# Kernel optimization log

Hardware: AMD Instinct MI355X
Metric: run time of the kernel (lower is better)

Reference implementation:

```python
import jax, jax.numpy as jnp
import numpy as np
import math

D_MODEL, N_HEADS, D_FF = 1024, 16, 4096
HEAD_DIM = D_MODEL // N_HEADS
BATCH, SEQ = 2, 2048
POPE_BASE = 10000.0
LN_EPS = 1e-5


def setup_inputs() -> dict:
    key = jax.random.key(0)
    ks = jax.random.split(key, 20)
    s = 0.02
    inp = {
        "x": jax.random.normal(ks[0], (BATCH, SEQ, D_MODEL), dtype=jnp.float32),
        "positions": jnp.arange(SEQ, dtype=jnp.int64) if jax.config.jax_enable_x64 else jnp.arange(SEQ, dtype=jnp.int32),
        "Wq": jax.random.normal(ks[1], (D_MODEL, D_MODEL), jnp.float32) * s,
        "bq": jnp.zeros((D_MODEL,), jnp.float32),
        "Wk": jax.random.normal(ks[2], (D_MODEL, D_MODEL), jnp.float32) * s,
        "bk": jnp.zeros((D_MODEL,), jnp.float32),
        "Wv": jax.random.normal(ks[3], (D_MODEL, D_MODEL), jnp.float32) * s,
        "bv": jnp.zeros((D_MODEL,), jnp.float32),
        "Wo": jax.random.normal(ks[4], (D_MODEL, D_MODEL), jnp.float32) * s,
        "bo": jnp.zeros((D_MODEL,), jnp.float32),
        "phase_bias": jax.random.uniform(ks[5], (N_HEADS, HEAD_DIM), jnp.float32,
                                          minval=-2.0 * math.pi, maxval=0.0),
        "freqs": (1.0 / POPE_BASE ** (jnp.arange(HEAD_DIM, dtype=jnp.float32) / HEAD_DIM)),
        "W1": jax.random.normal(ks[6], (D_MODEL, D_FF), jnp.float32) * s,
        "b1": jnp.zeros((D_FF,), jnp.float32),
        "W2": jax.random.normal(ks[7], (D_FF, D_MODEL), jnp.float32) * s,
        "b2": jnp.zeros((D_MODEL,), jnp.float32),
        "g1": jnp.ones((D_MODEL,), jnp.float32),
        "beta1": jnp.zeros((D_MODEL,), jnp.float32),
        "g2": jnp.ones((D_MODEL,), jnp.float32),
        "beta2": jnp.zeros((D_MODEL,), jnp.float32),
    }
    return inp


def _layernorm(x, g, b):
    mu = jnp.mean(x, axis=-1, keepdims=True)
    var = jnp.mean((x - mu) ** 2, axis=-1, keepdims=True)
    return (x - mu) * jax.lax.rsqrt(var + LN_EPS) * g + b


def reference(x, positions, Wq, bq, Wk, bk, Wv, bv, Wo, bo, phase_bias, freqs,
              W1, b1, W2, b2, g1, beta1, g2, beta2):
    B, S, D = x.shape
    H, hd = N_HEADS, HEAD_DIM

    def split_heads(y):  # (B,S,D) -> (B,H,S,hd)
        return y.reshape(B, S, H, hd).transpose(0, 2, 1, 3)

    q = split_heads(x @ Wq + bq)
    k = split_heads(x @ Wk + bk)
    v = split_heads(x @ Wv + bv)

    # --- PoPE: magnitudes via softplus, phases from positions + learned bias ---
    mu_q = jax.nn.softplus(q)
    mu_k = jax.nn.softplus(k)
    pos_phases = positions[:, None].astype(jnp.float32) * freqs[None, :]        # (S,hd)
    phases = pos_phases[None, None, :, :] + phase_bias[None, :, None, :]        # (1,H,S,hd)
    cosp, sinp = jnp.cos(phases), jnp.sin(phases)
    q_pope = jnp.concatenate([mu_q * cosp, mu_q * sinp], axis=-1)               # (B,H,S,2hd)
    k_pope = jnp.concatenate([mu_k * cosp, mu_k * sinp], axis=-1)

    # --- manual causal attention with softmax1 ---
    scale = 1.0 / math.sqrt(2 * hd)  # q.shape[-1] == 2*head_dim under PoPE
    scores = jnp.einsum("bhsd,bhtd->bhst", q_pope, k_pope) * scale
    causal = jnp.triu(jnp.ones((S, S), dtype=bool), k=1)
    scores = jnp.where(causal[None, None], -jnp.inf, scores)
    m = jnp.max(scores, axis=-1, keepdims=True)
    e = jnp.exp(scores - m)
    attn_w = e / (1.0 + jnp.sum(e, axis=-1, keepdims=True))  # softmax1 (as written in source)
    attn = jnp.einsum("bhst,bhtd->bhsd", attn_w, v)

    attn = attn.transpose(0, 2, 1, 3).reshape(B, S, D) @ Wo + bo
    x = _layernorm(x + attn, g1, beta1)
    ff = jax.nn.relu(x @ W1 + b1) @ W2 + b2
    x = _layernorm(x + ff, g2, beta2)
    return x
```

## Files before the change

### kernel.cpp

```cpp
#include <hip/hip_runtime.h>
#include <hip/hip_bf16.h>
#include <math.h>

#define B_   2
#define S_   2048
#define D_   1024
#define H_   16
#define HD_  64
#define DFF_ 4096
#define M_   (B_*S_)
#define SCALE_ 0.08838834764831845f

typedef __attribute__((ext_vector_type(8))) short bf16x8;
typedef __attribute__((ext_vector_type(4))) float f32x4;

#define MFMA16(a,b,c) __builtin_amdgcn_mfma_f32_16x16x32_bf16((a),(b),(c),0,0,0)

__device__ __forceinline__ unsigned short f2b(float f) {
    union { float f; unsigned u; } v; v.f = f;
    return (unsigned short)((v.u + 0x7FFFu + ((v.u >> 16) & 1u)) >> 16);
}
__device__ __forceinline__ float b2f(unsigned short s) {
    union { unsigned u; float f; } v; v.u = ((unsigned)s) << 16;
    return v.f;
}
__device__ __forceinline__ unsigned pk2bf(float a, float b) {
    union { float f; unsigned u; } ua, ub; ua.f = a; ub.f = b;
    return __builtin_amdgcn_perm(ub.u, ua.u, 0x07060302u);
}
__device__ __forceinline__ float softplus_f(float x) {
    return fmaxf(x, 0.f) + log1pf(__expf(-fabsf(x)));
}
__device__ __forceinline__ void g2l16(const void* g, void* l) {
    __builtin_amdgcn_global_load_lds(
        (const __attribute__((address_space(1))) unsigned int*)g,
        (__attribute__((address_space(3))) unsigned int*)l, 16, 0, 0);
}

__global__ __launch_bounds__(256) void conv_bf16_kernel(
    const float* __restrict__ in, unsigned short* __restrict__ out,
    const float* __restrict__ bq, const float* __restrict__ bk,
    const float* __restrict__ bv, float* __restrict__ bqkv)
{
    int i = (blockIdx.x * 256 + threadIdx.x) * 4;
    float4 v = *(const float4*)&in[i];
    ushort4 o;
    o.x = f2b(v.x); o.y = f2b(v.y); o.z = f2b(v.z); o.w = f2b(v.w);
    *(ushort4*)&out[i] = o;
    int j = blockIdx.x * 256 + threadIdx.x;
    if (j < 3072)
        bqkv[j] = (j < 1024) ? bq[j] : (j < 2048 ? bk[j - 1024] : bv[j - 2048]);
}

__global__ __launch_bounds__(256) void wtrans_kernel(
    const float* __restrict__ W, unsigned short* __restrict__ WT, int K, int N)
{
    __shared__ float tile[32][33];
    const int n0 = blockIdx.x * 32, k0 = blockIdx.y * 32;
    const int tx = threadIdx.x & 31, ty = threadIdx.x >> 5;
    #pragma unroll
    for (int i = 0; i < 4; i++)
        tile[ty + 8*i][tx] = W[(size_t)(k0 + ty + 8*i) * N + n0 + tx];
    __syncthreads();
    #pragma unroll
    for (int i = 0; i < 4; i++)
        WT[(size_t)(n0 + ty + 8*i) * K + k0 + tx] = f2b(tile[tx][ty + 8*i]);
}

__global__ __launch_bounds__(256) void wtrans4_kernel(
    const float* __restrict__ Wa, const float* __restrict__ Wb,
    const float* __restrict__ Wc, const float* __restrict__ Wd,
    unsigned short* __restrict__ Tabc, unsigned short* __restrict__ Td)
{
    __shared__ float tile[32][33];
    const int z = blockIdx.z;
    const float* W = (z == 0) ? Wa : (z == 1) ? Wb : (z == 2) ? Wc : Wd;
    unsigned short* WT = (z < 3) ? Tabc + (size_t)z * 1024 * 1024 : Td;
    const int n0 = blockIdx.x * 32, k0 = blockIdx.y * 32;
    const int tx = threadIdx.x & 31, ty = threadIdx.x >> 5;
    #pragma unroll
    for (int i = 0; i < 4; i++)
        tile[ty + 8*i][tx] = W[(size_t)(k0 + ty + 8*i) * 1024 + n0 + tx];
    __syncthreads();
    #pragma unroll
    for (int i = 0; i < 4; i++)
        WT[(size_t)(n0 + ty + 8*i) * 1024 + k0 + tx] = f2b(tile[tx][ty + 8*i]);
}

__global__ __launch_bounds__(256) void gemm_bf16_kernel(
    const unsigned short* __restrict__ A,
    const unsigned short* __restrict__ WT,
    const float* __restrict__ bias,
    float* __restrict__ outF, unsigned short* __restrict__ outB,
    int M, int Kslice, int lda, int N, int relu)
{
    __shared__ unsigned short As[2][128 * 64];
    __shared__ unsigned short Bs[2][128 * 64];

    const int tid = threadIdx.x;
    const int w = tid >> 6, lane = tid & 63;
    const int quad = lane >> 4, l16 = lane & 15;

    const int nn = gridDim.x, nm = gridDim.y;
    const int lin = ((int)blockIdx.z * nm + (int)blockIdx.y) * nn + (int)blockIdx.x;
    const int per = (nn * nm * (int)gridDim.z) >> 3;
    const int id  = (lin & 7) * per + (lin >> 3);
    const int zz  = id / (nn * nm);
    const int rem = id - zz * nn * nm;
    const int mt_ = rem / nn, nt_ = rem - mt_ * nn;

    const size_t m0 = (size_t)mt_ * 128, n0 = (size_t)nt_ * 128;
    const int wm = (w >> 1) * 64, wn = (w & 1) * 64;
    const int koff = zz * Kslice;

    const int srow = lane >> 3;
    const int sc   = ((lane & 7) ^ srow) * 8;
    const unsigned short* ga = A  + (m0 + w * 32 + srow) * (size_t)lda + koff + sc;
    const unsigned short* gb = WT + (n0 + w * 32 + srow) * (size_t)lda + koff + sc;
    const size_t rows8 = (size_t)8 * lda;

    f32x4 acc[4][4] = {};
    const int niter = Kslice >> 6;

    #pragma unroll
    for (int j = 0; j < 4; j++) g2l16(ga + j * rows8, &As[0][(w * 32 + j * 8) * 64]);
    #pragma unroll
    for (int j = 0; j < 4; j++) g2l16(gb + j * rows8, &Bs[0][(w * 32 + j * 8) * 64]);

    for (int i = 0; i < niter; i++) {
        __syncthreads();
        if (i + 1 < niter) {
            const int nb = (i + 1) & 1, k0 = (i + 1) << 6;
            #pragma unroll
            for (int j = 0; j < 4; j++)
                g2l16(ga + j * rows8 + k0, &As[nb][(w * 32 + j * 8) * 64]);
            #pragma unroll
            for (int j = 0; j < 4; j++)
                g2l16(gb + j * rows8 + k0, &Bs[nb][(w * 32 + j * 8) * 64]);
        }
        const int buf = i & 1;

        #pragma unroll
        for (int kk = 0; kk < 2; kk++) {
            bf16x8 af[4], bfr[4];
            #pragma unroll
            for (int t = 0; t < 4; t++) {
                const int slot = ((kk * 4 + quad) ^ (l16 & 7)) * 8;
                af[t]  = *(const bf16x8*)&As[buf][(wm + t * 16 + l16) * 64 + slot];
                bfr[t] = *(const bf16x8*)&Bs[buf][(wn + t * 16 + l16) * 64 + slot];
            }
            #pragma unroll
            for (int mt = 0; mt < 4; mt++)
                #pragma unroll
                for (int nt = 0; nt < 4; nt++)
                    acc[mt][nt] = MFMA16(af[mt], bfr[nt], acc[mt][nt]);
        }
    }

    float bv[4];
    #pragma unroll
    for (int nt = 0; nt < 4; nt++)
        bv[nt] = (zz == 0) ? bias[n0 + wn + nt * 16 + l16] : 0.f;

    float* outFz = outF ? outF + (size_t)zz * M * N : nullptr;

    #pragma unroll
    for (int mt = 0; mt < 4; mt++) {
        #pragma unroll
        for (int nt = 0; nt < 4; nt++) {
            const size_t n = n0 + wn + nt * 16 + l16;
            #pragma unroll
            for (int r = 0; r < 4; r++) {
                const size_t m = m0 + wm + mt * 16 + quad * 4 + r;
                float val = acc[mt][nt][r] + bv[nt];
                if (relu) val = fmaxf(val, 0.f);
                const size_t idx = m * N + n;
                if (outFz) outFz[idx] = val;
                if (outB) outB[idx] = f2b(val);
            }
        }
    }
}

__global__ __launch_bounds__(256) void pope_kernel(
    const unsigned short* __restrict__ qkv,
    const float* __restrict__ phase_bias, const float* __restrict__ freqs,
    unsigned short* __restrict__ qp, unsigned short* __restrict__ kp)
{
    int idx = blockIdx.x * 256 + threadIdx.x;
    int d = idx & 63;
    int s = (idx >> 6) & (S_ - 1);
    int h = (idx >> 17) & (H_ - 1);
    int b = idx >> 21;

    size_t src = (size_t)(b * S_ + s) * 3072 + h * HD_ + d;
    float muq = softplus_f(b2f(qkv[src])) * SCALE_;
    float muk = softplus_f(b2f(qkv[src + 1024]));

    float ph = (float)s * freqs[d] + phase_bias[h * HD_ + d];
    float sn, cs;
    __sincosf(ph, &sn, &cs);

    size_t o = ((size_t)(b * H_ + h) * S_ + s) * 128 + d;
    qp[o]      = f2b(muq * cs);
    qp[o + 64] = f2b(muq * sn);
    kp[o]      = f2b(muk * cs);
    kp[o + 64] = f2b(muk * sn);
}

__global__ __launch_bounds__(256) void vtrans_kernel(
    const unsigned short* __restrict__ qkv, unsigned short* __restrict__ vt)
{
    __shared__ unsigned short tile[64][72];
    const int bh = blockIdx.y, b = bh >> 4, h = bh & 15;
    const int s0 = blockIdx.x * 64;
    const int tid = threadIdx.x;
    #pragma unroll
    for (int i = 0; i < 16; i++) {
        int idx = i * 256 + tid;
        int s = idx >> 6, d = idx & 63;
        tile[s][d] = qkv[(size_t)(b * S_ + s0 + s) * 3072 + 2048 + h * HD_ + d];
    }
    __syncthreads();
    #pragma unroll
    for (int i = 0; i < 16; i++) {
        int idx = i * 256 + tid;
        int d = idx >> 6, s = idx & 63;
        vt[((size_t)bh * 64 + d) * S_ + s0 + s] = tile[s][d];
    }
}

__global__ __launch_bounds__(512, 4) void attn_mfma_kernel(
    const unsigned short* __restrict__ qp,
    const unsigned short* __restrict__ kp,
    const unsigned short* __restrict__ vt,
    unsigned short* __restrict__ ao)
{
    __shared__ unsigned short kt_lds[2][64][128];
    __shared__ unsigned short vt_lds[2][64][64];
    __shared__ unsigned short p_lds[8][16][72];

    const int tid = threadIdx.x;
    const int w = tid >> 6, lane = tid & 63;
    const int quad = lane >> 4, l16 = lane & 15;
    const int bh = blockIdx.y, b = bh >> 4, h = bh & 15;

    const int a = (blockIdx.z == 0) ? 15 - (int)blockIdx.x : (int)blockIdx.x;
    const int q0b = a * 128;
    const int q0 = q0b + w * 16;

    const unsigned short* qbase = qp + ((size_t)bh * S_ + q0 + l16) * 128 + quad * 8;
    bf16x8 qa[4];
    #pragma unroll
    for (int kc = 0; kc < 4; kc++) qa[kc] = *(const bf16x8*)(qbase + kc * 32);

    const int krow = lane >> 4, kslot = lane & 15;
    const int vrow = lane >> 3, vslot = lane & 7;
    const int kr0 = w * 8 + krow,     kc0 = kslot ^ (kr0 & 15);
    const int kr1 = w * 8 + 4 + krow, kc1 = kslot ^ (kr1 & 15);
    const int vd  = w * 8 + vrow,     vc  = vslot ^ (vd & 7);
    const unsigned short* kg0 = kp + ((size_t)bh * S_ + kr0) * 128 + kc0 * 8;
    const unsigned short* kg1 = kp + ((size_t)bh * S_ + kr1) * 128 + kc1 * 8;
    const unsigned short* vg0 = vt + ((size_t)bh * 64 + vd) * S_ + vc * 8;

    f32x4 o[4] = {};
    float ms = -1e30f, ls = 0.f;

    const int ntiles = 2 * a + 2;

    g2l16(kg0, &kt_lds[0][w * 8][0]);
    g2l16(kg1, &kt_lds[0][w * 8 + 4][0]);
    g2l16(vg0, &vt_lds[0][w * 8][0]);

    for (int ti = 0; ti < ntiles; ti++) {
        const int t0 = ti * 64;
        __syncthreads();
        if (ti + 1 < ntiles) {
            const int nb = (ti + 1) & 1;
            const size_t ko = (size_t)(ti + 1) * (64 * 128);
            const size_t vo = (size_t)(ti + 1) * 64;
            g2l16(kg0 + ko, &kt_lds[nb][w * 8][0]);
            g2l16(kg1 + ko, &kt_lds[nb][w * 8 + 4][0]);
            g2l16(vg0 + vo, &vt_lds[nb][w * 8][0]);
        }
        const int buf = ti & 1;

        if (t0 <= q0 + 15) {
            f32x4 sf[4];
            __builtin_amdgcn_s_setprio(1);
            #pragma unroll
            for (int kg = 0; kg < 4; kg++) {
                f32x4 s = {0, 0, 0, 0};
                const int row = kg * 16 + l16;
                #pragma unroll
                for (int kc = 0; kc < 4; kc++) {
                    const int slot = (kc * 4 + quad) ^ l16;
                    s = MFMA16(*(const bf16x8*)&kt_lds[buf][row][slot * 8], qa[kc], s);
                }
                sf[kg] = s;
            }
            __builtin_amdgcn_s_setprio(0);

            const int qrow = q0 + l16;
            const bool dmask = (t0 + 63 > q0);
            #pragma unroll
            for (int kg = 0; kg < 4; kg++) {
                const int kbase = t0 + kg * 16 + quad * 4;
                float v0 = sf[kg][0], v1 = sf[kg][1], v2 = sf[kg][2], v3 = sf[kg][3];
                if (dmask) {
                    v0 = (kbase     <= qrow) ? v0 : -1e30f;
                    v1 = (kbase + 1 <= qrow) ? v1 : -1e30f;
                    v2 = (kbase + 2 <= qrow) ? v2 : -1e30f;
                    v3 = (kbase + 3 <= qrow) ? v3 : -1e30f;
                }
                ms = fmaxf(ms, fmaxf(fmaxf(v0, v1), fmaxf(v2, v3)));
                const float e0 = __expf(v0), e1 = __expf(v1);
                const float e2 = __expf(v2), e3 = __expf(v3);
                ls += (e0 + e1) + (e2 + e3);
                uint2 pk;
                pk.x = pk2bf(e0, e1);
                pk.y = pk2bf(e2, e3);
                *(uint2*)&p_lds[w][l16][kg * 16 + quad * 4] = pk;
            }
            asm volatile("s_waitcnt lgkmcnt(0)" ::: "memory");
            bf16x8 pa0 = *(const bf16x8*)&p_lds[w][l16][quad * 8];
            bf16x8 pa1 = *(const bf16x8*)&p_lds[w][l16][quad * 8 + 32];

            __builtin_amdgcn_s_setprio(1);
            #pragma unroll
            for (int dg = 0; dg < 4; dg++) {
                const int row = dg * 16 + l16;
                const int s0_ = quad ^ (l16 & 7);
                const int s1_ = (quad + 4) ^ (l16 & 7);
                o[dg] = MFMA16(pa0, *(const bf16x8*)&vt_lds[buf][row][s0_ * 8], o[dg]);
                o[dg] = MFMA16(pa1, *(const bf16x8*)&vt_lds[buf][row][s1_ * 8], o[dg]);
            }
            __builtin_amdgcn_s_setprio(0);
        }
    }

    float mv = ms, lv = ls;
    mv = fmaxf(mv, __shfl_xor(mv, 16, 64)); lv += __shfl_xor(lv, 16, 64);
    mv = fmaxf(mv, __shfl_xor(mv, 32, 64)); lv += __shfl_xor(lv, 32, 64);
    const float inv = 1.f / (__expf(mv) + lv);

    #pragma unroll
    for (int r = 0; r < 4; r++) {
        const float ir = __shfl(inv, quad * 4 + r, 64);
        const int row = q0 + quad * 4 + r;
        const size_t base = (size_t)(b * S_ + row) * D_ + h * HD_ + l16;
        ao[base]      = f2b(o[0][r] * ir);
        ao[base + 16] = f2b(o[1][r] * ir);
        ao[base + 32] = f2b(o[2][r] * ir);
        ao[base + 48] = f2b(o[3][r] * ir);
    }
}

__global__ __launch_bounds__(256) void ln_kernel(
    const float* __restrict__ ya, const float* __restrict__ yb,
    const float* __restrict__ resF, const unsigned short* __restrict__ resB,
    const float* __restrict__ g, const float* __restrict__ beta,
    float* __restrict__ outF, unsigned short* __restrict__ outB)
{
    const int row = blockIdx.x;
    const int tid = threadIdx.x;
    const float* yr = ya + (size_t)row * D_;
    const float* y2 = yb ? yb + (size_t)row * D_ : nullptr;

    float t[4];
    float sum = 0.f, sumsq = 0.f;
    #pragma unroll
    for (int i = 0; i < 4; i++) {
        int c = tid + 256 * i;
        float rv = resF ? resF[(size_t)row * D_ + c] : b2f(resB[(size_t)row * D_ + c]);
        t[i] = yr[c] + rv + (y2 ? y2[c] : 0.f);
        sum += t[i]; sumsq += t[i] * t[i];
    }
    #pragma unroll
    for (int off = 32; off >= 1; off >>= 1) {
        sum   += __shfl_xor(sum,   off, 64);
        sumsq += __shfl_xor(sumsq, off, 64);
    }
    __shared__ float rs_[4], rq_[4];
    int w = tid >> 6, lane = tid & 63;
    if (lane == 0) { rs_[w] = sum; rq_[w] = sumsq; }
    __syncthreads();
    float tot  = rs_[0] + rs_[1] + rs_[2] + rs_[3];
    float totq = rq_[0] + rq_[1] + rq_[2] + rq_[3];
    float mu   = tot  * (1.f / D_);
    float var  = totq * (1.f / D_) - mu * mu;
    float rstd = rsqrtf(var + 1e-5f);

    #pragma unroll
    for (int i = 0; i < 4; i++) {
        int c = tid + 256 * i;
        float val = (t[i] - mu) * rstd * g[c] + beta[c];
        if (outF) outF[(size_t)row * D_ + c] = val;
        if (outB) outB[(size_t)row * D_ + c] = f2b(val);
    }
}

extern "C" void kernel_launch(void* const* d_in, const int* in_sizes, int n_in,
                              void* d_out, int out_size, void* d_ws, size_t ws_size,
                              hipStream_t stream)
{
    const float* x   = (const float*)d_in[0];
    const float* Wq  = (const float*)d_in[2];
    const float* bq  = (const float*)d_in[3];
    const float* Wk  = (const float*)d_in[4];
    const float* bk  = (const float*)d_in[5];
    const float* Wv  = (const float*)d_in[6];
    const float* bv  = (const float*)d_in[7];
    const float* Wo  = (const float*)d_in[8];
    const float* bo  = (const float*)d_in[9];
    const float* phase_bias = (const float*)d_in[10];
    const float* freqs = (const float*)d_in[11];
    const float* W1  = (const float*)d_in[12];
    const float* b1  = (const float*)d_in[13];
    const float* W2  = (const float*)d_in[14];
    const float* b2  = (const float*)d_in[15];
    const float* g1  = (const float*)d_in[16];
    const float* be1 = (const float*)d_in[17];
    const float* g2  = (const float*)d_in[18];
    const float* be2 = (const float*)d_in[19];
    float* out = (float*)d_out;

    char* base = (char*)d_ws;
    const size_t MiB = 1024 * 1024;
    unsigned short* WqkvT = (unsigned short*)(base);
    unsigned short* WoT   = (unsigned short*)(base + 6  * MiB);
    unsigned short* W1T   = (unsigned short*)(base + 8  * MiB);
    unsigned short* W2T   = (unsigned short*)(base + 16 * MiB);
    float*          bqkv  = (float*)(base + 24 * MiB);
    unsigned short* xb    = (unsigned short*)(base + 25 * MiB);
    unsigned short* qkvb  = (unsigned short*)(base + 33 * MiB);
    unsigned short* qpb   = (unsigned short*)(base + 57 * MiB);
    unsigned short* kpb   = (unsigned short*)(base + 73 * MiB);
    unsigned short* vtb   = (unsigned short*)(base + 89 * MiB);
    float*          po    = (float*)(base + 89 * MiB);
    unsigned short* aob   = xb;
    unsigned short* x1b   = xb;
    unsigned short* hb    = qkvb;
    float*          fo    = po;

    dim3 blk(256);

    conv_bf16_kernel<<<dim3(M_ * D_ / 1024), blk, 0, stream>>>(x, xb, bq, bk, bv, bqkv);
    wtrans4_kernel<<<dim3(32, 32, 4), blk, 0, stream>>>(Wq, Wk, Wv, Wo, WqkvT, WoT);
    wtrans_kernel<<<dim3(DFF_ / 32, D_ / 32), blk, 0, stream>>>(W1, W1T, D_, DFF_);
    wtrans_kernel<<<dim3(D_ / 32, DFF_ / 32), blk, 0, stream>>>(W2, W2T, DFF_, D_);

    gemm_bf16_kernel<<<dim3(3072 / 128, M_ / 128, 1), blk, 0, stream>>>(
        xb, WqkvT, bqkv, nullptr, qkvb, M_, D_, D_, 3072, 0);

    pope_kernel<<<dim3(B_ * H_ * S_ * HD_ / 256), blk, 0, stream>>>(
        qkvb, phase_bias, freqs, qpb, kpb);
    vtrans_kernel<<<dim3(S_ / 64, B_ * H_), blk, 0, stream>>>(qkvb, vtb);

    attn_mfma_kernel<<<dim3(8, B_ * H_, 2), dim3(512), 0, stream>>>(qpb, kpb, vtb, aob);

    gemm_bf16_kernel<<<dim3(D_ / 128, M_ / 128, 2), blk, 0, stream>>>(
        aob, WoT, bo, po, nullptr, M_, D_ / 2, D_, D_, 0);
    ln_kernel<<<dim3(M_), blk, 0, stream>>>(
        po, po + (size_t)M_ * D_, x, nullptr, g1, be1, nullptr, x1b);

    gemm_bf16_kernel<<<dim3(DFF_ / 128, M_ / 128, 1), blk, 0, stream>>>(
        x1b, W1T, b1, nullptr, hb, M_, D_, D_, DFF_, 1);
    gemm_bf16_kernel<<<dim3(D_ / 128, M_ / 128, 2), blk, 0, stream>>>(
        hb, W2T, b2, fo, nullptr, M_, DFF_ / 2, DFF_, D_, 0);
    ln_kernel<<<dim3(M_), blk, 0, stream>>>(
        fo, fo + (size_t)M_ * D_, nullptr, x1b, g2, be2, out, nullptr);
}
```

Before: 397.8 us.

## Vectorize pope/vtrans/layernorm and pass attention P through shuffles instead of LDS

The pope, V-transpose and layernorm kernels now move four elements per thread with ushort4/float4 loads and stores, which cuts the number of memory instructions in these bandwidth-bound passes. The attention kernel drops its LDS staging buffer for the probability tile and rebuilds the MFMA A operand with cross-lane shuffles, freeing shared memory so launch_bounds can ask for 6 blocks per CU instead of 4. It also removes the s_setprio hints. The shuffle path adds VALU and permute work per tile, and the higher occupancy target may increase register pressure.

```diff
diff --git a/kernel.cpp b/kernel.cpp
--- a/kernel.cpp
+++ b/kernel.cpp
@@ -188,49 +188,78 @@
     unsigned short* __restrict__ qp, unsigned short* __restrict__ kp)
 {
     int idx = blockIdx.x * 256 + threadIdx.x;
-    int d = idx & 63;
-    int s = (idx >> 6) & (S_ - 1);
-    int h = (idx >> 17) & (H_ - 1);
-    int b = idx >> 21;
-
-    size_t src = (size_t)(b * S_ + s) * 3072 + h * HD_ + d;
-    float muq = softplus_f(b2f(qkv[src])) * SCALE_;
-    float muk = softplus_f(b2f(qkv[src + 1024]));
-
-    float ph = (float)s * freqs[d] + phase_bias[h * HD_ + d];
-    float sn, cs;
-    __sincosf(ph, &sn, &cs);
-
-    size_t o = ((size_t)(b * H_ + h) * S_ + s) * 128 + d;
-    qp[o]      = f2b(muq * cs);
-    qp[o + 64] = f2b(muq * sn);
-    kp[o]      = f2b(muk * cs);
-    kp[o + 64] = f2b(muk * sn);
+    int d4 = (idx & 15) * 4;
+    int s  = (idx >> 4) & (S_ - 1);
+    int h  = (idx >> 15) & (H_ - 1);
+    int b  = idx >> 19;
+
+    size_t src = (size_t)(b * S_ + s) * 3072 + h * HD_ + d4;
+    ushort4 qv = *(const ushort4*)&qkv[src];
+    ushort4 kv = *(const ushort4*)&qkv[src + 1024];
+    float4 fr = *(const float4*)&freqs[d4];
+    float4 pb = *(const float4*)&phase_bias[h * HD_ + d4];
+    const float fs = (float)s;
+
+    ushort4 qc4, qs4, kc4, ks4;
+    {
+        float muq = softplus_f(b2f(qv.x)) * SCALE_, muk = softplus_f(b2f(kv.x));
+        float sn, cs; __sincosf(fs * fr.x + pb.x, &sn, &cs);
+        qc4.x = f2b(muq * cs); qs4.x = f2b(muq * sn);
+        kc4.x = f2b(muk * cs); ks4.x = f2b(muk * sn);
+    }
+    {
+        float muq = softplus_f(b2f(qv.y)) * SCALE_, muk = softplus_f(b2f(kv.y));
+        float sn, cs; __sincosf(fs * fr.y + pb.y, &sn, &cs);
+        qc4.y = f2b(muq * cs); qs4.y = f2b(muq * sn);
+        kc4.y = f2b(muk * cs); ks4.y = f2b(muk * sn);
+    }
+    {
+        float muq = softplus_f(b2f(qv.z)) * SCALE_, muk = softplus_f(b2f(kv.z));
+        float sn, cs; __sincosf(fs * fr.z + pb.z, &sn, &cs);
+        qc4.z = f2b(muq * cs); qs4.z = f2b(muq * sn);
+        kc4.z = f2b(muk * cs); ks4.z = f2b(muk * sn);
+    }
+    {
+        float muq = softplus_f(b2f(qv.w)) * SCALE_, muk = softplus_f(b2f(kv.w));
+        float sn, cs; __sincosf(fs * fr.w + pb.w, &sn, &cs);
+        qc4.w = f2b(muq * cs); qs4.w = f2b(muq * sn);
+        kc4.w = f2b(muk * cs); ks4.w = f2b(muk * sn);
+    }
+
+    size_t o = ((size_t)(b * H_ + h) * S_ + s) * 128 + d4;
+    *(ushort4*)&qp[o]      = qc4;
+    *(ushort4*)&qp[o + 64] = qs4;
+    *(ushort4*)&kp[o]      = kc4;
+    *(ushort4*)&kp[o + 64] = ks4;
 }
 
 __global__ __launch_bounds__(256) void vtrans_kernel(
     const unsigned short* __restrict__ qkv, unsigned short* __restrict__ vt)
 {
-    __shared__ unsigned short tile[64][72];
+    __shared__ unsigned short tile[64][68];
     const int bh = blockIdx.y, b = bh >> 4, h = bh & 15;
     const int s0 = blockIdx.x * 64;
     const int tid = threadIdx.x;
     #pragma unroll
-    for (int i = 0; i < 16; i++) {
+    for (int i = 0; i < 4; i++) {
         int idx = i * 256 + tid;
-        int s = idx >> 6, d = idx & 63;
-        tile[s][d] = qkv[(size_t)(b * S_ + s0 + s) * 3072 + 2048 + h * HD_ + d];
+        int s = idx >> 4, d4 = (idx & 15) * 4;
+        *(ushort4*)&tile[s][d4] =
+            *(const ushort4*)&qkv[(size_t)(b * S_ + s0 + s) * 3072 + 2048 + h * HD_ + d4];
     }
     __syncthreads();
     #pragma unroll
-    for (int i = 0; i < 16; i++) {
+    for (int i = 0; i < 4; i++) {
         int idx = i * 256 + tid;
-        int d = idx >> 6, s = idx & 63;
-        vt[((size_t)bh * 64 + d) * S_ + s0 + s] = tile[s][d];
-    }
-}
-
-__global__ __launch_bounds__(512, 4) void attn_mfma_kernel(
+        int d = idx >> 4, s4 = (idx & 15) * 4;
+        ushort4 o;
+        o.x = tile[s4][d]; o.y = tile[s4 + 1][d];
+        o.z = tile[s4 + 2][d]; o.w = tile[s4 + 3][d];
+        *(ushort4*)&vt[((size_t)bh * 64 + d) * S_ + s0 + s4] = o;
+    }
+}
+
+__global__ __launch_bounds__(512, 6) void attn_mfma_kernel(
     const unsigned short* __restrict__ qp,
     const unsigned short* __restrict__ kp,
     const unsigned short* __restrict__ vt,
@@ -238,7 +267,6 @@
 {
     __shared__ unsigned short kt_lds[2][64][128];
     __shared__ unsigned short vt_lds[2][64][64];
-    __shared__ unsigned short p_lds[8][16][72];
 
     const int tid = threadIdx.x;
     const int w = tid >> 6, lane = tid & 63;
@@ -287,7 +315,6 @@
 
         if (t0 <= q0 + 15) {
             f32x4 sf[4];
-            __builtin_amdgcn_s_setprio(1);
             #pragma unroll
             for (int kg = 0; kg < 4; kg++) {
                 f32x4 s = {0, 0, 0, 0};
@@ -299,10 +326,10 @@
                 }
                 sf[kg] = s;
             }
-            __builtin_amdgcn_s_setprio(0);
 
             const int qrow = q0 + l16;
             const bool dmask = (t0 + 63 > q0);
+            unsigned pk8[8];
             #pragma unroll
             for (int kg = 0; kg < 4; kg++) {
                 const int kbase = t0 + kg * 16 + quad * 4;
@@ -317,16 +344,28 @@
                 const float e0 = __expf(v0), e1 = __expf(v1);
                 const float e2 = __expf(v2), e3 = __expf(v3);
                 ls += (e0 + e1) + (e2 + e3);
-                uint2 pk;
-                pk.x = pk2bf(e0, e1);
-                pk.y = pk2bf(e2, e3);
-                *(uint2*)&p_lds[w][l16][kg * 16 + quad * 4] = pk;
+                pk8[kg * 2]     = pk2bf(e0, e1);
+                pk8[kg * 2 + 1] = pk2bf(e2, e3);
             }
-            asm volatile("s_waitcnt lgkmcnt(0)" ::: "memory");
-            bf16x8 pa0 = *(const bf16x8*)&p_lds[w][l16][quad * 8];
-            bf16x8 pa1 = *(const bf16x8*)&p_lds[w][l16][quad * 8 + 32];
-
-            __builtin_amdgcn_s_setprio(1);
+
+            const int sA = ((quad & 1) << 5) + l16;
+            const int sB = sA + 16;
+            unsigned sa0 = __shfl(pk8[0], sA, 64), sa1 = __shfl(pk8[1], sA, 64);
+            unsigned sa2 = __shfl(pk8[2], sA, 64), sa3 = __shfl(pk8[3], sA, 64);
+            unsigned sa4 = __shfl(pk8[4], sA, 64), sa5 = __shfl(pk8[5], sA, 64);
+            unsigned sa6 = __shfl(pk8[6], sA, 64), sa7 = __shfl(pk8[7], sA, 64);
+            unsigned sb0 = __shfl(pk8[0], sB, 64), sb1 = __shfl(pk8[1], sB, 64);
+            unsigned sb2 = __shfl(pk8[2], sB, 64), sb3 = __shfl(pk8[3], sB, 64);
+            unsigned sb4 = __shfl(pk8[4], sB, 64), sb5 = __shfl(pk8[5], sB, 64);
+            unsigned sb6 = __shfl(pk8[6], sB, 64), sb7 = __shfl(pk8[7], sB, 64);
+            const bool hi = quad >= 2;
+            union { unsigned u[4]; bf16x8 v; } pa0u, pa1u;
+            pa0u.u[0] = hi ? sa2 : sa0;  pa0u.u[1] = hi ? sa3 : sa1;
+            pa0u.u[2] = hi ? sb2 : sb0;  pa0u.u[3] = hi ? sb3 : sb1;
+            pa1u.u[0] = hi ? sa6 : sa4;  pa1u.u[1] = hi ? sa7 : sa5;
+            pa1u.u[2] = hi ? sb6 : sb4;  pa1u.u[3] = hi ? sb7 : sb5;
+            const bf16x8 pa0 = pa0u.v, pa1 = pa1u.v;
+
             #pragma unroll
             for (int dg = 0; dg < 4; dg++) {
                 const int row = dg * 16 + l16;
@@ -335,7 +374,6 @@
                 o[dg] = MFMA16(pa0, *(const bf16x8*)&vt_lds[buf][row][s0_ * 8], o[dg]);
                 o[dg] = MFMA16(pa1, *(const bf16x8*)&vt_lds[buf][row][s1_ * 8], o[dg]);
             }
-            __builtin_amdgcn_s_setprio(0);
         }
     }
 
@@ -364,18 +402,24 @@
 {
     const int row = blockIdx.x;
     const int tid = threadIdx.x;
-    const float* yr = ya + (size_t)row * D_;
-    const float* y2 = yb ? yb + (size_t)row * D_ : nullptr;
-
-    float t[4];
-    float sum = 0.f, sumsq = 0.f;
-    #pragma unroll
-    for (int i = 0; i < 4; i++) {
-        int c = tid + 256 * i;
-        float rv = resF ? resF[(size_t)row * D_ + c] : b2f(resB[(size_t)row * D_ + c]);
-        t[i] = yr[c] + rv + (y2 ? y2[c] : 0.f);
-        sum += t[i]; sumsq += t[i] * t[i];
-    }
+    const int c = tid * 4;
+    const size_t base = (size_t)row * D_ + c;
+
+    float4 t4 = *(const float4*)(ya + base);
+    if (yb) {
+        float4 y4 = *(const float4*)(yb + base);
+        t4.x += y4.x; t4.y += y4.y; t4.z += y4.z; t4.w += y4.w;
+    }
+    if (resF) {
+        float4 r4 = *(const float4*)(resF + base);
+        t4.x += r4.x; t4.y += r4.y; t4.z += r4.z; t4.w += r4.w;
+    } else {
+        ushort4 r4 = *(const ushort4*)(resB + base);
+        t4.x += b2f(r4.x); t4.y += b2f(r4.y); t4.z += b2f(r4.z); t4.w += b2f(r4.w);
+    }
+    float sum   = (t4.x + t4.y) + (t4.z + t4.w);
+    float sumsq = (t4.x * t4.x + t4.y * t4.y) + (t4.z * t4.z + t4.w * t4.w);
+
     #pragma unroll
     for (int off = 32; off >= 1; off >>= 1) {
         sum   += __shfl_xor(sum,   off, 64);
@@ -391,12 +435,18 @@
     float var  = totq * (1.f / D_) - mu * mu;
     float rstd = rsqrtf(var + 1e-5f);
 
-    #pragma unroll
-    for (int i = 0; i < 4; i++) {
-        int c = tid + 256 * i;
-        float val = (t[i] - mu) * rstd * g[c] + beta[c];
-        if (outF) outF[(size_t)row * D_ + c] = val;
-        if (outB) outB[(size_t)row * D_ + c] = f2b(val);
+    float4 g4 = *(const float4*)(g + c);
+    float4 b4 = *(const float4*)(beta + c);
+    float4 o4;
+    o4.x = (t4.x - mu) * rstd * g4.x + b4.x;
+    o4.y = (t4.y - mu) * rstd * g4.y + b4.y;
+    o4.z = (t4.z - mu) * rstd * g4.z + b4.z;
+    o4.w = (t4.w - mu) * rstd * g4.w + b4.w;
+    if (outF) *(float4*)(outF + base) = o4;
+    if (outB) {
+        ushort4 ob;
+        ob.x = f2b(o4.x); ob.y = f2b(o4.y); ob.z = f2b(o4.z); ob.w = f2b(o4.w);
+        *(ushort4*)(outB + base) = ob;
     }
 }
 
@@ -453,7 +503,7 @@
     gemm_bf16_kernel<<<dim3(3072 / 128, M_ / 128, 1), blk, 0, stream>>>(
         xb, WqkvT, bqkv, nullptr, qkvb, M_, D_, D_, 3072, 0);
 
-    pope_kernel<<<dim3(B_ * H_ * S_ * HD_ / 256), blk, 0, stream>>>(
+    pope_kernel<<<dim3(B_ * H_ * S_ * 16 / 256), blk, 0, stream>>>(
         qkvb, phase_bias, freqs, qpb, kpb);
     vtrans_kernel<<<dim3(S_ / 64, B_ * H_), blk, 0, stream>>>(qkvb, vtb);
 
```

Measured after the change: 392.2 us. No clear change (-1.4%).
